# Kernel tuning notes

Measured on AMD Instinct MI355X. Metric: run time of the kernel, lower is better.

The kernel has to match this reference:

```python
import jax, jax.numpy as jnp
import numpy as np

ALPHA = 1.5      # entmax parameter from __init__
N_ITER = 50      # bisection iterations (converges well past fp32 precision)


def entmax_bisect(x, alpha=ALPHA, n_iter=N_ITER):
    """alpha-entmax along the last axis via bisection on the threshold tau.
    p_i = ((alpha-1)*x_i - tau)_+ ** (1/(alpha-1)), with sum_i p_i = 1.
    """
    q = 1.0 / (alpha - 1.0)
    z = x * (alpha - 1.0)
    mx = jnp.max(z, axis=-1, keepdims=True)
    # tau is bracketed by [mx - 1, mx]: sum >= 1 at lo, sum = 0 at hi
    lo, hi = mx - 1.0, mx

    def body(_, carry):
        lo, hi = carry
        tau = 0.5 * (lo + hi)
        f = jnp.sum(jnp.maximum(z - tau, 0.0) ** q, axis=-1, keepdims=True) - 1.0
        lo = jnp.where(f > 0.0, tau, lo)
        hi = jnp.where(f > 0.0, hi, tau)
        return lo, hi

    lo, hi = jax.lax.fori_loop(0, n_iter, body, (lo, hi))
    tau = 0.5 * (lo + hi)
    p = jnp.maximum(z - tau, 0.0) ** q
    return p / jnp.sum(p, axis=-1, keepdims=True)  # exact renormalization


def setup_inputs() -> dict:
    key = jax.random.key(0)
    kq, kk, kv = jax.random.split(key, 3)
    B, T, D = 16, 2048, 256
    return {
        "query": jax.random.normal(kq, (B, T, D), dtype=jnp.float32),
        "value": jax.random.normal(kv, (B, T, D), dtype=jnp.float32),
        "key": jax.random.normal(kk, (B, T, D), dtype=jnp.float32),
    }


def reference(query, value, key):
    # scores: [B, Tq, Tk]
    scores = jnp.einsum("btd,bsd->bts", query, key)
    weights = entmax_bisect(scores)          # sparse attention weights
    return jnp.einsum("bts,bsd->btd", weights, value)
```

## Files before the change

kernel.cpp:

```cpp
#include <hip/hip_runtime.h>

#define TT 2048
#define DD 256
#define RQB 128
#define NT 512
#define KB 128
#define NTILE (TT / KB)
#define NITER 30
#define CAP 28

#define L_CIDX 131072
#define L_CVAL (L_CIDX + RQB * CAP * 2)
#define L_CNT  (L_CVAL + RQB * CAP * 4)
#define L_SLOT (L_CNT + RQB * 4)
#define L_OVF  (L_SLOT + 8 * 16 * CAP * 2)
#define LDS_SZ (L_OVF + 16)

typedef __attribute__((ext_vector_type(4))) float f32x4;
typedef __attribute__((ext_vector_type(8))) short short8;

__device__ inline unsigned short f2bf(float x) {
    unsigned u = __float_as_uint(x);
    return (unsigned short)((u + 0x7fffu + ((u >> 16) & 1u)) >> 16);
}
__device__ inline float bf2f(unsigned short h) {
    return __uint_as_float((unsigned)h << 16);
}

__device__ __forceinline__ void gload16(const void* g, void* l) {
    __builtin_amdgcn_global_load_lds(
        (const __attribute__((address_space(1))) void*)g,
        (__attribute__((address_space(3))) void*)l, 16, 0, 0);
}

__device__ __forceinline__ float dppmax16(float m) {
    int a = __builtin_amdgcn_update_dpp(__float_as_int(m), __float_as_int(m),
                                        0xB1, 0xF, 0xF, false);
    m = fmaxf(m, __int_as_float(a));
    a = __builtin_amdgcn_update_dpp(__float_as_int(m), __float_as_int(m),
                                    0x4E, 0xF, 0xF, false);
    m = fmaxf(m, __int_as_float(a));
    a = __builtin_amdgcn_update_dpp(__float_as_int(m), __float_as_int(m),
                                    0x141, 0xF, 0xF, false);
    m = fmaxf(m, __int_as_float(a));
    a = __builtin_amdgcn_update_dpp(__float_as_int(m), __float_as_int(m),
                                    0x140, 0xF, 0xF, false);
    m = fmaxf(m, __int_as_float(a));
    return m;
}

__global__ __launch_bounds__(256) void split_k_kernel(const float* __restrict__ K,
        unsigned short* __restrict__ Kh, int n4) {
    int i = blockIdx.x * 256 + threadIdx.x;
    const int stride = gridDim.x * 256;
    for (; i < n4; i += stride) {
        float4 v = ((const float4*)K)[i];
        unsigned short h0 = f2bf(0.5f * v.x), h1 = f2bf(0.5f * v.y);
        unsigned short h2 = f2bf(0.5f * v.z), h3 = f2bf(0.5f * v.w);
        uint2 hv;
        hv.x = (unsigned)h0 | ((unsigned)h1 << 16);
        hv.y = (unsigned)h2 | ((unsigned)h3 << 16);
        ((uint2*)Kh)[i] = hv;
    }
}

__launch_bounds__(NT, 2)
__global__ void entmax_screen_kernel(const float* __restrict__ Q,
                                     const unsigned short* __restrict__ Kh,
                                     const float* __restrict__ Kf,
                                     const float* __restrict__ V,
                                     float* __restrict__ Out,
                                     int nwg) {
    extern __shared__ char smem[];
    unsigned short* CIDX = (unsigned short*)(smem + L_CIDX);
    float*          CVAL = (float*)(smem + L_CVAL);
    int*            CNT  = (int*)(smem + L_CNT);
    unsigned short* SLOT = (unsigned short*)(smem + L_SLOT);
    int*            POVF = (int*)(smem + L_OVF);

    const int tid = threadIdx.x;
    const int wid = tid >> 6, lane = tid & 63;
    const int l15 = lane & 15, ag = lane >> 4;
    const int wrow0 = wid * 16;

    const int lb = (blockIdx.x & 7) * (nwg >> 3) + (blockIdx.x >> 3);
    const int b  = lb >> 4;
    const int t0 = (lb & 15) * RQB;

    const char* KhB = (const char*)(Kh + (size_t)b * TT * DD);

    if (tid == 0) *POVF = 0;

    short8 ah[8];
    {
        const float* qr = Q + (size_t)(b * TT + t0 + wrow0 + l15) * DD;
        #pragma unroll
        for (int kk = 0; kk < 8; ++kk) {
            const int d0 = kk * 32 + ag * 8;
            float4 qa = *(const float4*)(qr + d0);
            float4 qb = *(const float4*)(qr + d0 + 4);
            float qf[8] = {qa.x, qa.y, qa.z, qa.w, qb.x, qb.y, qb.z, qb.w};
            #pragma unroll
            for (int i = 0; i < 8; ++i) ah[kk][i] = (short)f2bf(qf[i]);
        }
    }

    auto STAGE = [&](int tile, int buf) {
        #pragma unroll
        for (int j = 0; j < 8; ++j) {
            const int ofs = wid * 8192 + j * 1024 + lane * 16;
            const int cl = ofs >> 9, wb = ofs & 511;
            const size_t gb = ((size_t)((tile << 7) + cl) << 9) +
                              (size_t)(wb ^ ((cl & 7) << 4));
            gload16(KhB + gb, smem + buf * 65536 + wid * 8192 + j * 1024);
        }
    };

    STAGE(0, 0);
    __syncthreads();

    const unsigned long long grpmask = 0xFFFFULL << (ag * 16);
    const unsigned long long lowmask = (lane == 0) ? 0ULL : ((~0ULL) >> (64 - lane));
    float rmax[4];
    int   base[4];
    #pragma unroll
    for (int r = 0; r < 4; ++r) { rmax[r] = -3.402823466e38f; base[r] = 0; }

    for (int t = 0; t < NTILE; ++t) {
        const int cur = t & 1;
        if (t + 1 < NTILE) STAGE(t + 1, cur ^ 1);
        f32x4 acc[8];
        #pragma unroll
        for (int ct = 0; ct < 8; ++ct)
            #pragma unroll
            for (int r = 0; r < 4; ++r) acc[ct][r] = 0.0f;
        #pragma unroll
        for (int kk = 0; kk < 8; ++kk) {
            short8 bh[8];
            #pragma unroll
            for (int ct = 0; ct < 8; ++ct)
                bh[ct] = *(const short8*)(smem + cur * 65536 + (ct * 16 + l15) * 512 +
                                          (((kk * 64) + ag * 16) ^ ((l15 & 7) << 4)));
            #pragma unroll
            for (int ct = 0; ct < 8; ++ct)
                acc[ct] = __builtin_amdgcn_mfma_f32_16x16x32_bf16(ah[kk], bh[ct], acc[ct], 0, 0, 0);
        }
        #pragma unroll
        for (int rg = 0; rg < 4; ++rg) {
            float m = acc[0][rg];
            #pragma unroll
            for (int ct = 1; ct < 8; ++ct) m = fmaxf(m, acc[ct][rg]);
            m = dppmax16(m);
            rmax[rg] = fmaxf(rmax[rg], m);
            const float thr = rmax[rg] - 1.6f;
            if (m > thr) {
                const int row = wrow0 + ag * 4 + rg;
                #pragma unroll
                for (int ct = 0; ct < 8; ++ct) {
                    const bool p = acc[ct][rg] > thr;
                    const unsigned long long ball = __ballot(p) & grpmask;
                    if (ball) {
                        const int rank = (int)__popcll(ball & lowmask);
                        if (p && base[rg] + rank < CAP)
                            CIDX[row * CAP + base[rg] + rank] =
                                (unsigned short)((t << 7) + ct * 16 + l15);
                        base[rg] += (int)__popcll(ball);
                    }
                }
            }
        }
        __syncthreads();
    }

    #pragma unroll
    for (int rg = 0; rg < 4; ++rg) {
        if (l15 == 0) {
            CNT[wrow0 + ag * 4 + rg] = base[rg];
            if (base[rg] > CAP) *POVF = 1;
        }
    }
    __syncthreads();

    int c = 0;
    if (lane < 16) {
        const int cc = CNT[wrow0 + lane];
        c = cc > CAP ? CAP : cc;
    }
    int x = c;
    #pragma unroll
    for (int off = 1; off < 16; off <<= 1) {
        const int v = __shfl_up(x, off);
        if ((lane & 15) >= off) x += v;
    }
    const int pfx = x - c;
    const int total = __shfl(x, 15);
    if (lane < 16)
        for (int i = 0; i < c; ++i)
            SLOT[wid * (16 * CAP) + pfx + i] = (unsigned short)((lane << 8) | i);
    __syncthreads();

    {
        const float* Qb = Q + (size_t)(b * TT + t0 + wrow0) * DD;
        const float* Kb = Kf + (size_t)b * TT * DD;
        for (int bs = 0; bs < total; bs += 8) {
            float4 qv[8], kv[8];
            int rl[8], ii[8];
            #pragma unroll
            for (int u = 0; u < 8; ++u) {
                const int s = bs + u;
                const int e = (s < total) ? (int)SLOT[wid * (16 * CAP) + s] : 0;
                rl[u] = e >> 8; ii[u] = e & 255;
                const int col = (s < total) ? (int)CIDX[(wrow0 + rl[u]) * CAP + ii[u]] : 0;
                qv[u] = *(const float4*)(Qb + (size_t)rl[u] * DD + lane * 4);
                kv[u] = *(const float4*)(Kb + (size_t)col * DD + lane * 4);
            }
            float sm[8];
            #pragma unroll
            for (int u = 0; u < 8; ++u) {
                float d = qv[u].x * kv[u].x;
                d = fmaf(qv[u].y, kv[u].y, d);
                d = fmaf(qv[u].z, kv[u].z, d);
                d = fmaf(qv[u].w, kv[u].w, d);
                sm[u] = d;
            }
            #pragma unroll
            for (int off = 32; off; off >>= 1)
                #pragma unroll
                for (int u = 0; u < 8; ++u) sm[u] += __shfl_xor(sm[u], off);
            #pragma unroll
            for (int u = 0; u < 8; ++u)
                if (lane == u && bs + u < total)
                    CVAL[(wrow0 + rl[u]) * CAP + ii[u]] = 0.5f * sm[u];
        }
    }
    __syncthreads();

    if (*POVF) {
        if (wid == 0) {
            float* fbz = (float*)smem;
            for (int r = 0; r < RQB; ++r) {
                if (CNT[r] <= CAP) continue;
                const float* qr = Q + (size_t)(b * TT + t0 + r) * DD;
                const float* Kb = Kf + (size_t)b * TT * DD;
                for (int cc2 = lane; cc2 < TT; cc2 += 64) {
                    const float* kr = Kb + (size_t)cc2 * DD;
                    float a = 0.0f;
                    for (int d = 0; d < DD; ++d) a = fmaf(qr[d], kr[d], a);
                    fbz[cc2] = 0.5f * a;
                }
                __threadfence_block();
                float m = -3.402823466e38f;
                for (int cc2 = lane; cc2 < TT; cc2 += 64) m = fmaxf(m, fbz[cc2]);
                #pragma unroll
                for (int off = 32; off; off >>= 1) m = fmaxf(m, __shfl_xor(m, off));
                float lo = m - 1.0f, hi = m, tau;
                for (int it = 0; it < NITER; ++it) {
                    tau = 0.5f * (lo + hi);
                    float s = 0.0f;
                    for (int cc2 = lane; cc2 < TT; cc2 += 64) {
                        const float tt2 = fmaxf(fbz[cc2] - tau, 0.0f);
                        s = fmaf(tt2, tt2, s);
                    }
                    #pragma unroll
                    for (int off = 32; off; off >>= 1) s += __shfl_xor(s, off);
                    const bool gt = s > 1.0f;
                    lo = gt ? tau : lo;
                    hi = gt ? hi : tau;
                }
                tau = 0.5f * (lo + hi);
                float ssum = 0.0f;
                for (int cc2 = lane; cc2 < TT; cc2 += 64) {
                    const float tt2 = fmaxf(fbz[cc2] - tau, 0.0f);
                    ssum = fmaf(tt2, tt2, ssum);
                }
                #pragma unroll
                for (int off = 32; off; off >>= 1) ssum += __shfl_xor(ssum, off);
                const float inv = 1.0f / ssum;
                const int d4 = lane * 4;
                float4 o = make_float4(0.f, 0.f, 0.f, 0.f);
                for (int s = 0; s < TT; ++s) {
                    const float tt2 = fmaxf(fbz[s] - tau, 0.0f);
                    const float w = tt2 * tt2 * inv;
                    if (w > 0.0f) {
                        const float4 v = *(const float4*)(V + ((size_t)b * TT + s) * DD + d4);
                        o.x = fmaf(w, v.x, o.x); o.y = fmaf(w, v.y, o.y);
                        o.z = fmaf(w, v.z, o.z); o.w = fmaf(w, v.w, o.w);
                    }
                }
                *(float4*)(Out + ((size_t)(b * TT + t0 + r)) * DD + d4) = o;
                if (lane == 0) CNT[r] = -1;
                __threadfence_block();
            }
        }
        __syncthreads();
    }

    {
        const int myrow = wrow0 + (lane & 15);
        const int nRaw = CNT[myrow];
        const int n = (nRaw < 0) ? 0 : (nRaw > CAP ? CAP : nRaw);
        float cvr[CAP];
        #pragma unroll
        for (int i = 0; i < CAP; ++i)
            cvr[i] = (i < n) ? CVAL[myrow * CAP + i] : -3.0e30f;
        float emax = cvr[0];
        #pragma unroll
        for (int i = 1; i < CAP; ++i) emax = fmaxf(emax, cvr[i]);
        float lo = emax - 1.0f, hi = emax;
        for (int it = 0; it < NITER; ++it) {
            const float tau = 0.5f * (lo + hi);
            float s = 0.0f;
            #pragma unroll
            for (int i = 0; i < CAP; ++i) {
                const float tt2 = fmaxf(cvr[i] - tau, 0.0f);
                s = fmaf(tt2, tt2, s);
            }
            const bool gt = s > 1.0f;
            lo = gt ? tau : lo;
            hi = gt ? hi : tau;
        }
        const float tau = 0.5f * (lo + hi);
        float ssum = 0.0f;
        #pragma unroll
        for (int i = 0; i < CAP; ++i) {
            const float tt2 = fmaxf(cvr[i] - tau, 0.0f);
            ssum = fmaf(tt2, tt2, ssum);
        }
        const float inv = 1.0f / ssum;
        if (lane < 16 && n > 0) {
            for (int i = 0; i < n; ++i) {
                const float tt2 = fmaxf(cvr[i] - tau, 0.0f);
                CVAL[myrow * CAP + i] = tt2 * tt2 * inv;
            }
        }
    }

    const float* Vb = V + (size_t)b * TT * DD;
    for (int j = 0; j < 16; ++j) {
        const int row = wrow0 + j;
        const int n = CNT[row];
        if (n < 0) continue;
        const int d4 = lane * 4;
        float4 o = make_float4(0.f, 0.f, 0.f, 0.f);
        for (int i = 0; i < n; ++i) {
            const float wi = CVAL[row * CAP + i];
            if (wi > 0.0f) {
                const int si = (int)CIDX[row * CAP + i];
                const float4 v = *(const float4*)(Vb + (size_t)si * DD + d4);
                o.x = fmaf(wi, v.x, o.x); o.y = fmaf(wi, v.y, o.y);
                o.z = fmaf(wi, v.z, o.z); o.w = fmaf(wi, v.w, o.w);
            }
        }
        *(float4*)(Out + ((size_t)(b * TT + t0 + row)) * DD + d4) = o;
    }
}

#define DOT4(A, Kv, Qv) \
    A = fmaf((Qv).x, (Kv).x, fmaf((Qv).y, (Kv).y, fmaf((Qv).z, (Kv).z, fmaf((Qv).w, (Kv).w, (A)))))

__launch_bounds__(256, 2)
__global__ void entmax_fallback_kernel(const float* __restrict__ Q,
                                       const float* __restrict__ V,
                                       const float* __restrict__ K,
                                       float* __restrict__ Out) {
    extern __shared__ float zshf[];
    const int tid = threadIdx.x;
    const int b   = blockIdx.x >> 8;
    const int t0  = (blockIdx.x & 255) * 8;
    const float* Qb = Q + ((size_t)b * TT + t0) * DD;
    const float* Kb = K + (size_t)b * TT * DD;
    const float* Vb = V + (size_t)b * TT * DD;
    for (int g = 0; g < 2; ++g) {
        const int c0 = (g << 10) + tid;
        const float* k0 = Kb + (size_t)c0 * DD;
        float4 acc[8];
        #pragma unroll
        for (int r = 0; r < 8; ++r) acc[r] = make_float4(0.f, 0.f, 0.f, 0.f);
        for (int d = 0; d < DD; d += 4) {
            const float4 ka = *(const float4*)(k0 + d);
            const float4 kb = *(const float4*)(k0 + 256 * DD + d);
            const float4 kc = *(const float4*)(k0 + 512 * DD + d);
            const float4 kd = *(const float4*)(k0 + 768 * DD + d);
            #pragma unroll
            for (int r = 0; r < 8; ++r) {
                const float4 qv = *(const float4*)(Qb + r * DD + d);
                DOT4(acc[r].x, ka, qv); DOT4(acc[r].y, kb, qv);
                DOT4(acc[r].z, kc, qv); DOT4(acc[r].w, kd, qv);
            }
        }
        #pragma unroll
        for (int r = 0; r < 8; ++r) {
            zshf[r * TT + c0      ] = 0.5f * acc[r].x;
            zshf[r * TT + c0 + 256] = 0.5f * acc[r].y;
            zshf[r * TT + c0 + 512] = 0.5f * acc[r].z;
            zshf[r * TT + c0 + 768] = 0.5f * acc[r].w;
        }
    }
    __syncthreads();
    {
        const int wid = tid >> 6, lane = tid & 63;
        for (int rr = 0; rr < 2; ++rr) {
            const int r = wid * 2 + rr;
            float* z = zshf + r * TT;
            float zv[32];
            float m = -3.402823466e38f;
            #pragma unroll
            for (int j = 0; j < 32; ++j) { zv[j] = z[lane + (j << 6)]; m = fmaxf(m, zv[j]); }
            #pragma unroll
            for (int off = 32; off; off >>= 1) m = fmaxf(m, __shfl_xor(m, off));
            float lo = m - 1.0f, hi = m;
            for (int it = 0; it < NITER; ++it) {
                const float tau = 0.5f * (lo + hi);
                float s = 0.f;
                #pragma unroll
                for (int j = 0; j < 32; ++j) { float t = fmaxf(zv[j] - tau, 0.f); s = fmaf(t, t, s); }
                #pragma unroll
                for (int off = 32; off; off >>= 1) s += __shfl_xor(s, off);
                const bool gt = (s - 1.0f) > 0.0f;
                lo = gt ? tau : lo; hi = gt ? hi : tau;
            }
            const float tau = 0.5f * (lo + hi);
            float ssum = 0.f;
            #pragma unroll
            for (int j = 0; j < 32; ++j) { float t = fmaxf(zv[j] - tau, 0.f); ssum = fmaf(t, t, ssum); }
            #pragma unroll
            for (int off = 32; off; off >>= 1) ssum += __shfl_xor(ssum, off);
            const float inv = 1.0f / ssum;
            #pragma unroll
            for (int j = 0; j < 32; ++j) {
                float t = fmaxf(zv[j] - tau, 0.f);
                z[lane + (j << 6)] = t * t * inv;
            }
        }
    }
    __syncthreads();
    {
        const int d2 = (tid & 127) * 2;
        const int sg = tid >> 7;
        float2 acc[8];
        #pragma unroll
        for (int r = 0; r < 8; ++r) acc[r] = make_float2(0.f, 0.f);
        for (int sc = 0; sc < TT; sc += 8) {
            const int s0 = sc + sg * 4;
            float4 w4[8];
            #pragma unroll
            for (int r = 0; r < 8; ++r) w4[r] = *(const float4*)&zshf[r * TT + s0];
            #pragma unroll
            for (int js = 0; js < 4; ++js) {
                const float2 v = *(const float2*)(Vb + (size_t)(s0 + js) * DD + d2);
                #pragma unroll
                for (int r = 0; r < 8; ++r) {
                    const float wv = (js == 0) ? w4[r].x : (js == 1) ? w4[r].y
                                   : (js == 2) ? w4[r].z : w4[r].w;
                    acc[r].x = fmaf(wv, v.x, acc[r].x);
                    acc[r].y = fmaf(wv, v.y, acc[r].y);
                }
            }
        }
        __syncthreads();
        float* part = zshf;
        if (sg == 1) {
            #pragma unroll
            for (int r = 0; r < 8; ++r) *(float2*)&part[r * DD + d2] = acc[r];
        }
        __syncthreads();
        if (sg == 0) {
            #pragma unroll
            for (int r = 0; r < 8; ++r) {
                const float2 p = *(const float2*)&part[r * DD + d2];
                float2 o; o.x = acc[r].x + p.x; o.y = acc[r].y + p.y;
                *(float2*)&Out[((size_t)b * TT + t0 + r) * DD + d2] = o;
            }
        }
    }
}

extern "C" void kernel_launch(void* const* d_in, const int* in_sizes, int n_in,
                              void* d_out, int out_size, void* d_ws, size_t ws_size,
                              hipStream_t stream) {
    const float* Q = (const float*)d_in[0];
    const float* V = (const float*)d_in[1];
    const float* K = (const float*)d_in[2];
    float* Out = (float*)d_out;
    const int B = in_sizes[0] / (TT * DD);
    const size_t NE = (size_t)B * TT * DD;
    const size_t need = NE * 2;

    if (ws_size < need) {
        entmax_fallback_kernel<<<dim3(B * (TT / 8)), 256, 8 * TT * sizeof(float), stream>>>(
            Q, V, K, Out);
        return;
    }

    unsigned short* Kh = (unsigned short*)d_ws;
    split_k_kernel<<<2048, 256, 0, stream>>>(K, Kh, (int)(NE / 4));

    const int nwg = B * (TT / RQB);
    (void)hipFuncSetAttribute((const void*)entmax_screen_kernel,
                              hipFuncAttributeMaxDynamicSharedMemorySize, LDS_SZ);
    entmax_screen_kernel<<<dim3(nwg), NT, LDS_SZ, stream>>>(Q, Kh, K, V, Out, nwg);
}
```

Baseline: 135.0 us.

## Shrink workgroups to 32 query rows and 32-key tiles with precomputed LDS addressing

Cuts each workgroup from 128 query rows and 8 waves to 32 rows and 2 waves, with 32-key K tiles, so the grid has four times as many workgroups. The inner score loop now keeps two MFMA accumulators instead of eight. Global and LDS staging offsets and swizzled read pointers are computed once, before the loop. This aims for finer-grained scheduling and lower register and LDS pressure, but each workgroup still streams all of K, so total K traffic through L2 and the number of barriers per row rise.

```diff
diff --git a/kernel.cpp b/kernel.cpp
--- a/kernel.cpp
+++ b/kernel.cpp
@@ -2,18 +2,18 @@
 
 #define TT 2048
 #define DD 256
-#define RQB 128
-#define NT 512
-#define KB 128
+#define RQB 32
+#define NT 128
+#define KB 32
 #define NTILE (TT / KB)
 #define NITER 30
 #define CAP 28
 
-#define L_CIDX 131072
+#define L_CIDX 32768
 #define L_CVAL (L_CIDX + RQB * CAP * 2)
 #define L_CNT  (L_CVAL + RQB * CAP * 4)
 #define L_SLOT (L_CNT + RQB * 4)
-#define L_OVF  (L_SLOT + 8 * 16 * CAP * 2)
+#define L_OVF  (L_SLOT + 2 * 16 * CAP * 2)
 #define LDS_SZ (L_OVF + 16)
 
 typedef __attribute__((ext_vector_type(4))) float f32x4;
@@ -84,8 +84,8 @@
     const int wrow0 = wid * 16;
 
     const int lb = (blockIdx.x & 7) * (nwg >> 3) + (blockIdx.x >> 3);
-    const int b  = lb >> 4;
-    const int t0 = (lb & 15) * RQB;
+    const int b  = lb >> 6;
+    const int t0 = (lb & 63) * RQB;
 
     const char* KhB = (const char*)(Kh + (size_t)b * TT * DD);
 
@@ -105,18 +105,22 @@
         }
     }
 
-    auto STAGE = [&](int tile, int buf) {
-        #pragma unroll
-        for (int j = 0; j < 8; ++j) {
-            const int ofs = wid * 8192 + j * 1024 + lane * 16;
-            const int cl = ofs >> 9, wb = ofs & 511;
-            const size_t gb = ((size_t)((tile << 7) + cl) << 9) +
-                              (size_t)(wb ^ ((cl & 7) << 4));
-            gload16(KhB + gb, smem + buf * 65536 + wid * 8192 + j * 1024);
-        }
-    };
-
-    STAGE(0, 0);
+    int gofs[8], lofs[8];
+    #pragma unroll
+    for (int j = 0; j < 8; ++j) {
+        const int ofs = wid * 8192 + j * 1024 + lane * 16;
+        const int cl = ofs >> 9, wb = ofs & 511;
+        gofs[j] = cl * 512 + (wb ^ ((cl & 7) << 4));
+        lofs[j] = ofs;
+    }
+
+    const int sw = (l15 & 7) << 4;
+    const int qb_ = l15 * 512 + ((ag * 16) ^ (sw & 0x30));
+    const char* pE = smem + qb_ + (sw & 0x40);
+    const char* pO = smem + qb_ + (64 ^ (sw & 0x40));
+
+    #pragma unroll
+    for (int j = 0; j < 8; ++j) gload16(KhB + gofs[j], smem + lofs[j]);
     __syncthreads();
 
     const unsigned long long grpmask = 0xFFFFULL << (ag * 16);
@@ -128,42 +132,52 @@
 
     for (int t = 0; t < NTILE; ++t) {
         const int cur = t & 1;
-        if (t + 1 < NTILE) STAGE(t + 1, cur ^ 1);
-        f32x4 acc[8];
-        #pragma unroll
-        for (int ct = 0; ct < 8; ++ct)
-            #pragma unroll
-            for (int r = 0; r < 4; ++r) acc[ct][r] = 0.0f;
+        if (t + 1 < NTILE) {
+            const size_t gt = (size_t)(t + 1) * 16384;
+            const int lb_ = (cur ^ 1) * 16384;
+            #pragma unroll
+            for (int j = 0; j < 8; ++j)
+                gload16(KhB + gt + gofs[j], smem + lb_ + lofs[j]);
+        }
+        const char* pEc = pE + cur * 16384;
+        const char* pOc = pO + cur * 16384;
+        f32x4 acc0, acc1;
+        #pragma unroll
+        for (int r = 0; r < 4; ++r) { acc0[r] = 0.0f; acc1[r] = 0.0f; }
         #pragma unroll
         for (int kk = 0; kk < 8; ++kk) {
-            short8 bh[8];
-            #pragma unroll
-            for (int ct = 0; ct < 8; ++ct)
-                bh[ct] = *(const short8*)(smem + cur * 65536 + (ct * 16 + l15) * 512 +
-                                          (((kk * 64) + ag * 16) ^ ((l15 & 7) << 4)));
-            #pragma unroll
-            for (int ct = 0; ct < 8; ++ct)
-                acc[ct] = __builtin_amdgcn_mfma_f32_16x16x32_bf16(ah[kk], bh[ct], acc[ct], 0, 0, 0);
+            const char* pk = (kk & 1) ? pOc : pEc;
+            const short8 b0 = *(const short8*)(pk + (kk >> 1) * 128);
+            const short8 b1 = *(const short8*)(pk + 8192 + (kk >> 1) * 128);
+            acc0 = __builtin_amdgcn_mfma_f32_16x16x32_bf16(ah[kk], b0, acc0, 0, 0, 0);
+            acc1 = __builtin_amdgcn_mfma_f32_16x16x32_bf16(ah[kk], b1, acc1, 0, 0, 0);
         }
         #pragma unroll
         for (int rg = 0; rg < 4; ++rg) {
-            float m = acc[0][rg];
-            #pragma unroll
-            for (int ct = 1; ct < 8; ++ct) m = fmaxf(m, acc[ct][rg]);
-            m = dppmax16(m);
+            float m = dppmax16(fmaxf(acc0[rg], acc1[rg]));
             rmax[rg] = fmaxf(rmax[rg], m);
             const float thr = rmax[rg] - 1.6f;
             if (m > thr) {
                 const int row = wrow0 + ag * 4 + rg;
-                #pragma unroll
-                for (int ct = 0; ct < 8; ++ct) {
-                    const bool p = acc[ct][rg] > thr;
+                {
+                    const bool p = acc0[rg] > thr;
                     const unsigned long long ball = __ballot(p) & grpmask;
                     if (ball) {
                         const int rank = (int)__popcll(ball & lowmask);
                         if (p && base[rg] + rank < CAP)
                             CIDX[row * CAP + base[rg] + rank] =
-                                (unsigned short)((t << 7) + ct * 16 + l15);
+                                (unsigned short)((t << 5) + l15);
+                        base[rg] += (int)__popcll(ball);
+                    }
+                }
+                {
+                    const bool p = acc1[rg] > thr;
+                    const unsigned long long ball = __ballot(p) & grpmask;
+                    if (ball) {
+                        const int rank = (int)__popcll(ball & lowmask);
+                        if (p && base[rg] + rank < CAP)
+                            CIDX[row * CAP + base[rg] + rank] =
+                                (unsigned short)((t << 5) + 16 + l15);
                         base[rg] += (int)__popcll(ball);
                     }
                 }
```

Result: slower. 463.7 us (+243.5%).

## Split key columns across waves and screen candidates in two barrier-free passes

Applied to the files above, without the earlier changes.

Replaces the tile loop, in which all waves share double-buffered LDS K tiles with a barrier per tile, by a scheme where Q is staged once in LDS and each wave owns 256 key columns, reading K straight from global into registers. A first pass computes per-row maxima, which are reduced across waves into exact thresholds. A second pass recomputes the scores and collects candidates into per-wave lists (CAPW=6) that are then merged into the row list (CAP=24). This removes the 16 per-tile barriers and the running-max threshold, at the cost of computing QK^T twice. Tighter per-wave caps send more rows to the overflow path.

```diff
diff --git a/kernel.cpp b/kernel.cpp
--- a/kernel.cpp
+++ b/kernel.cpp
@@ -4,12 +4,16 @@
 #define DD 256
 #define RQB 128
 #define NT 512
-#define KB 128
-#define NTILE (TT / KB)
 #define NITER 30
-#define CAP 28
-
-#define L_CIDX 131072
+#define CAPW 6
+#define CAP 24
+#define THR_SLACK 1.75f
+
+#define L_GP   65536
+#define L_THR  (L_GP + 4096)
+#define L_CW   (L_THR + 512)
+#define L_IW   (L_CW + 4096)
+#define L_CIDX (L_IW + 8 * 128 * CAPW * 2)
 #define L_CVAL (L_CIDX + RQB * CAP * 2)
 #define L_CNT  (L_CVAL + RQB * CAP * 4)
 #define L_SLOT (L_CNT + RQB * 4)
@@ -25,12 +29,6 @@
 }
 __device__ inline float bf2f(unsigned short h) {
     return __uint_as_float((unsigned)h << 16);
-}
-
-__device__ __forceinline__ void gload16(const void* g, void* l) {
-    __builtin_amdgcn_global_load_lds(
-        (const __attribute__((address_space(1))) void*)g,
-        (__attribute__((address_space(3))) void*)l, 16, 0, 0);
 }
 
 __device__ __forceinline__ float dppmax16(float m) {
@@ -65,13 +63,17 @@
 }
 
 __launch_bounds__(NT, 2)
-__global__ void entmax_screen_kernel(const float* __restrict__ Q,
-                                     const unsigned short* __restrict__ Kh,
-                                     const float* __restrict__ Kf,
-                                     const float* __restrict__ V,
-                                     float* __restrict__ Out,
-                                     int nwg) {
+__global__ void entmax_nobar_kernel(const float* __restrict__ Q,
+                                    const unsigned short* __restrict__ Kh,
+                                    const float* __restrict__ Kf,
+                                    const float* __restrict__ V,
+                                    float* __restrict__ Out,
+                                    int nwg) {
     extern __shared__ char smem[];
+    float*          GP   = (float*)(smem + L_GP);
+    float*          THR  = (float*)(smem + L_THR);
+    int*            CW   = (int*)(smem + L_CW);
+    unsigned short* IW   = (unsigned short*)(smem + L_IW);
     unsigned short* CIDX = (unsigned short*)(smem + L_CIDX);
     float*          CVAL = (float*)(smem + L_CVAL);
     int*            CNT  = (int*)(smem + L_CNT);
@@ -89,102 +91,173 @@
 
     const char* KhB = (const char*)(Kh + (size_t)b * TT * DD);
 
+    ((int*)(smem + L_CW))[tid] = 0;
+    ((int*)(smem + L_CW))[tid + 512] = 0;
     if (tid == 0) *POVF = 0;
 
-    short8 ah[8];
     {
-        const float* qr = Q + (size_t)(b * TT + t0 + wrow0 + l15) * DD;
-        #pragma unroll
-        for (int kk = 0; kk < 8; ++kk) {
-            const int d0 = kk * 32 + ag * 8;
-            float4 qa = *(const float4*)(qr + d0);
-            float4 qb = *(const float4*)(qr + d0 + 4);
-            float qf[8] = {qa.x, qa.y, qa.z, qa.w, qb.x, qb.y, qb.z, qb.w};
-            #pragma unroll
-            for (int i = 0; i < 8; ++i) ah[kk][i] = (short)f2bf(qf[i]);
-        }
-    }
-
-    auto STAGE = [&](int tile, int buf) {
+        const int qrow = tid >> 2, seg = tid & 3;
+        const float* qsrc = Q + (size_t)(b * TT + t0 + qrow) * DD + seg * 64;
+        char* qd = smem + qrow * 512;
+        const int swr = (qrow & 7) << 4;
         #pragma unroll
         for (int j = 0; j < 8; ++j) {
-            const int ofs = wid * 8192 + j * 1024 + lane * 16;
-            const int cl = ofs >> 9, wb = ofs & 511;
-            const size_t gb = ((size_t)((tile << 7) + cl) << 9) +
-                              (size_t)(wb ^ ((cl & 7) << 4));
-            gload16(KhB + gb, smem + buf * 65536 + wid * 8192 + j * 1024);
-        }
-    };
-
-    STAGE(0, 0);
+            float4 f0 = *(const float4*)(qsrc + j * 8);
+            float4 f1 = *(const float4*)(qsrc + j * 8 + 4);
+            uint4 pk;
+            pk.x = (unsigned)f2bf(f0.x) | ((unsigned)f2bf(f0.y) << 16);
+            pk.y = (unsigned)f2bf(f0.z) | ((unsigned)f2bf(f0.w) << 16);
+            pk.z = (unsigned)f2bf(f1.x) | ((unsigned)f2bf(f1.y) << 16);
+            pk.w = (unsigned)f2bf(f1.z) | ((unsigned)f2bf(f1.w) << 16);
+            *(uint4*)(qd + ((seg * 128 + j * 16) ^ swr)) = pk;
+        }
+    }
     __syncthreads();
 
     const unsigned long long grpmask = 0xFFFFULL << (ag * 16);
     const unsigned long long lowmask = (lane == 0) ? 0ULL : ((~0ULL) >> (64 - lane));
-    float rmax[4];
-    int   base[4];
+    const int colw0 = wid * 256;
+    const int sx = (l15 & 7) << 4;
+    const char* qbase = smem + l15 * 512;
+
+    float mr[32];
     #pragma unroll
-    for (int r = 0; r < 4; ++r) { rmax[r] = -3.402823466e38f; base[r] = 0; }
-
-    for (int t = 0; t < NTILE; ++t) {
-        const int cur = t & 1;
-        if (t + 1 < NTILE) STAGE(t + 1, cur ^ 1);
-        f32x4 acc[8];
-        #pragma unroll
-        for (int ct = 0; ct < 8; ++ct)
-            #pragma unroll
-            for (int r = 0; r < 4; ++r) acc[ct][r] = 0.0f;
-        #pragma unroll
-        for (int kk = 0; kk < 8; ++kk) {
-            short8 bh[8];
-            #pragma unroll
-            for (int ct = 0; ct < 8; ++ct)
-                bh[ct] = *(const short8*)(smem + cur * 65536 + (ct * 16 + l15) * 512 +
-                                          (((kk * 64) + ag * 16) ^ ((l15 & 7) << 4)));
-            #pragma unroll
-            for (int ct = 0; ct < 8; ++ct)
-                acc[ct] = __builtin_amdgcn_mfma_f32_16x16x32_bf16(ah[kk], bh[ct], acc[ct], 0, 0, 0);
-        }
-        #pragma unroll
-        for (int rg = 0; rg < 4; ++rg) {
-            float m = acc[0][rg];
-            #pragma unroll
-            for (int ct = 1; ct < 8; ++ct) m = fmaxf(m, acc[ct][rg]);
-            m = dppmax16(m);
-            rmax[rg] = fmaxf(rmax[rg], m);
-            const float thr = rmax[rg] - 1.6f;
-            if (m > thr) {
-                const int row = wrow0 + ag * 4 + rg;
-                #pragma unroll
-                for (int ct = 0; ct < 8; ++ct) {
-                    const bool p = acc[ct][rg] > thr;
-                    const unsigned long long ball = __ballot(p) & grpmask;
-                    if (ball) {
-                        const int rank = (int)__popcll(ball & lowmask);
-                        if (p && base[rg] + rank < CAP)
-                            CIDX[row * CAP + base[rg] + rank] =
-                                (unsigned short)((t << 7) + ct * 16 + l15);
-                        base[rg] += (int)__popcll(ball);
+    for (int i = 0; i < 32; ++i) mr[i] = -3.0e30f;
+
+    for (int tc = 0; tc < 8; ++tc) {
+        const char* kb0 = KhB + (size_t)(colw0 + tc * 32 + l15) * 512 + ag * 16;
+        short8 Bf[2][8];
+        #pragma unroll
+        for (int ct = 0; ct < 2; ++ct)
+            #pragma unroll
+            for (int kk = 0; kk < 8; ++kk)
+                Bf[ct][kk] = *(const short8*)(kb0 + ct * 8192 + kk * 64);
+        #pragma unroll
+        for (int rp = 0; rp < 4; ++rp) {
+            f32x4 acc[2][2];
+            #pragma unroll
+            for (int rg = 0; rg < 2; ++rg)
+                #pragma unroll
+                for (int ct = 0; ct < 2; ++ct)
+                    #pragma unroll
+                    for (int r = 0; r < 4; ++r) acc[rg][ct][r] = 0.0f;
+            #pragma unroll
+            for (int kk = 0; kk < 8; ++kk) {
+                const int kb = (kk * 64 + ag * 16) ^ sx;
+                short8 a0 = *(const short8*)(qbase + (rp * 32) * 512 + kb);
+                short8 a1 = *(const short8*)(qbase + (rp * 32 + 16) * 512 + kb);
+                acc[0][0] = __builtin_amdgcn_mfma_f32_16x16x32_bf16(a0, Bf[0][kk], acc[0][0], 0, 0, 0);
+                acc[0][1] = __builtin_amdgcn_mfma_f32_16x16x32_bf16(a0, Bf[1][kk], acc[0][1], 0, 0, 0);
+                acc[1][0] = __builtin_amdgcn_mfma_f32_16x16x32_bf16(a1, Bf[0][kk], acc[1][0], 0, 0, 0);
+                acc[1][1] = __builtin_amdgcn_mfma_f32_16x16x32_bf16(a1, Bf[1][kk], acc[1][1], 0, 0, 0);
+            }
+            #pragma unroll
+            for (int rg = 0; rg < 2; ++rg)
+                #pragma unroll
+                for (int r = 0; r < 4; ++r)
+                    mr[rp * 8 + rg * 4 + r] = fmaxf(mr[rp * 8 + rg * 4 + r],
+                                                    fmaxf(acc[rg][0][r], acc[rg][1][r]));
+        }
+    }
+    #pragma unroll
+    for (int rp = 0; rp < 4; ++rp)
+        #pragma unroll
+        for (int rg = 0; rg < 2; ++rg)
+            #pragma unroll
+            for (int r = 0; r < 4; ++r) {
+                const float m = dppmax16(mr[rp * 8 + rg * 4 + r]);
+                if (l15 == 0)
+                    GP[wid * 128 + rp * 32 + rg * 16 + ag * 4 + r] = m;
+            }
+    __syncthreads();
+    if (tid < 128) {
+        float m = GP[tid];
+        #pragma unroll
+        for (int w = 1; w < 8; ++w) m = fmaxf(m, GP[w * 128 + tid]);
+        THR[tid] = m - THR_SLACK;
+    }
+    __syncthreads();
+
+    #pragma unroll
+    for (int rp = 0; rp < 4; ++rp)
+        #pragma unroll
+        for (int rg = 0; rg < 2; ++rg)
+            #pragma unroll
+            for (int r = 0; r < 4; ++r)
+                mr[rp * 8 + rg * 4 + r] = THR[rp * 32 + rg * 16 + ag * 4 + r];
+
+    for (int tc = 0; tc < 8; ++tc) {
+        const char* kb0 = KhB + (size_t)(colw0 + tc * 32 + l15) * 512 + ag * 16;
+        short8 Bf[2][8];
+        #pragma unroll
+        for (int ct = 0; ct < 2; ++ct)
+            #pragma unroll
+            for (int kk = 0; kk < 8; ++kk)
+                Bf[ct][kk] = *(const short8*)(kb0 + ct * 8192 + kk * 64);
+        #pragma unroll
+        for (int rp = 0; rp < 4; ++rp) {
+            f32x4 acc[2][2];
+            #pragma unroll
+            for (int rg = 0; rg < 2; ++rg)
+                #pragma unroll
+                for (int ct = 0; ct < 2; ++ct)
+                    #pragma unroll
+                    for (int r = 0; r < 4; ++r) acc[rg][ct][r] = 0.0f;
+            #pragma unroll
+            for (int kk = 0; kk < 8; ++kk) {
+                const int kb = (kk * 64 + ag * 16) ^ sx;
+                short8 a0 = *(const short8*)(qbase + (rp * 32) * 512 + kb);
+                short8 a1 = *(const short8*)(qbase + (rp * 32 + 16) * 512 + kb);
+                acc[0][0] = __builtin_amdgcn_mfma_f32_16x16x32_bf16(a0, Bf[0][kk], acc[0][0], 0, 0, 0);
+                acc[0][1] = __builtin_amdgcn_mfma_f32_16x16x32_bf16(a0, Bf[1][kk], acc[0][1], 0, 0, 0);
+                acc[1][0] = __builtin_amdgcn_mfma_f32_16x16x32_bf16(a1, Bf[0][kk], acc[1][0], 0, 0, 0);
+                acc[1][1] = __builtin_amdgcn_mfma_f32_16x16x32_bf16(a1, Bf[1][kk], acc[1][1], 0, 0, 0);
+            }
+            #pragma unroll
+            for (int rg = 0; rg < 2; ++rg)
+                #pragma unroll
+                for (int r = 0; r < 4; ++r) {
+                    const float thrv = mr[rp * 8 + rg * 4 + r];
+                    const int row = rp * 32 + rg * 16 + ag * 4 + r;
+                    #pragma unroll
+                    for (int ct = 0; ct < 2; ++ct) {
+                        const bool p = acc[rg][ct][r] > thrv;
+                        const unsigned long long ball = __ballot(p) & grpmask;
+                        if (ball) {
+                            const int cnt = (int)__popcll(ball);
+                            const int rank = (int)__popcll(ball & lowmask);
+                            const int base = CW[wid * 128 + row];
+                            if (p && base + rank < CAPW)
+                                IW[(wid * 128 + row) * CAPW + base + rank] =
+                                    (unsigned short)(colw0 + tc * 32 + ct * 16 + l15);
+                            if (l15 == 0) CW[wid * 128 + row] = base + cnt;
+                        }
                     }
                 }
-            }
-        }
-        __syncthreads();
-    }
-
-    #pragma unroll
-    for (int rg = 0; rg < 4; ++rg) {
-        if (l15 == 0) {
-            CNT[wrow0 + ag * 4 + rg] = base[rg];
-            if (base[rg] > CAP) *POVF = 1;
-        }
-    }
-    __syncthreads();
+        }
+    }
+    __syncthreads();
+
+    if (lane < 16) {
+        const int row = wrow0 + lane;
+        int n = 0, ovf = 0;
+        for (int w = 0; w < 8; ++w) {
+            int cw = CW[w * 128 + row];
+            if (cw > CAPW) { ovf = 1; cw = CAPW; }
+            for (int i = 0; i < cw; ++i) {
+                if (n < CAP) CIDX[row * CAP + n] = IW[(w * 128 + row) * CAPW + i];
+                ++n;
+            }
+        }
+        if (n > CAP) ovf = 1;
+        CNT[row] = ovf ? (CAP + 1) : n;
+        if (ovf) *POVF = 1;
+    }
 
     int c = 0;
     if (lane < 16) {
         const int cc = CNT[wrow0 + lane];
-        c = cc > CAP ? CAP : cc;
+        c = (cc > CAP) ? 0 : cc;
     }
     int x = c;
     #pragma unroll
@@ -197,7 +270,6 @@
     if (lane < 16)
         for (int i = 0; i < c; ++i)
             SLOT[wid * (16 * CAP) + pfx + i] = (unsigned short)((lane << 8) | i);
-    __syncthreads();
 
     {
         const float* Qb = Q + (size_t)(b * TT + t0 + wrow0) * DD;
@@ -298,7 +370,7 @@
     {
         const int myrow = wrow0 + (lane & 15);
         const int nRaw = CNT[myrow];
-        const int n = (nRaw < 0) ? 0 : (nRaw > CAP ? CAP : nRaw);
+        const int n = (nRaw < 0 || nRaw > CAP) ? 0 : nRaw;
         float cvr[CAP];
         #pragma unroll
         for (int i = 0; i < CAP; ++i)
@@ -339,7 +411,7 @@
     for (int j = 0; j < 16; ++j) {
         const int row = wrow0 + j;
         const int n = CNT[row];
-        if (n < 0) continue;
+        if (n < 0 || n > CAP) continue;
         const int d4 = lane * 4;
         float4 o = make_float4(0.f, 0.f, 0.f, 0.f);
         for (int i = 0; i < n; ++i) {
@@ -496,7 +568,7 @@
     split_k_kernel<<<2048, 256, 0, stream>>>(K, Kh, (int)(NE / 4));
 
     const int nwg = B * (TT / RQB);
-    (void)hipFuncSetAttribute((const void*)entmax_screen_kernel,
+    (void)hipFuncSetAttribute((const void*)entmax_nobar_kernel,
                               hipFuncAttributeMaxDynamicSharedMemorySize, LDS_SZ);
-    entmax_screen_kernel<<<dim3(nwg), NT, LDS_SZ, stream>>>(Q, Kh, K, V, Out, nwg);
-}
+    entmax_nobar_kernel<<<dim3(nwg), NT, LDS_SZ, stream>>>(Q, Kh, K, V, Out, nwg);
+}
```

After: 198.1 us. +46.8%, slower.

## Pack K in MFMA fragment layout and stream it from global directly into registers

Applied to the files above, without the earlier changes.

The K bf16 pre-pass now writes K in the exact per-lane MFMA B-fragment order, so the screening kernel loads B operands straight from global/L2 into registers. This drops the LDS double-buffered staging and its per-tile barriers. Work is regrouped so each wave covers 32 query rows over half the key columns, reusing each B fragment for two A fragments, and per-wave candidate lists are merged into a larger per-row CAP. It frees a large amount of LDS and removes synchronization, at the cost of more global/L2 traffic per wave and larger candidate buffers.

```diff
diff --git a/kernel.cpp b/kernel.cpp
--- a/kernel.cpp
+++ b/kernel.cpp
@@ -4,12 +4,15 @@
 #define DD 256
 #define RQB 128
 #define NT 512
-#define KB 128
-#define NTILE (TT / KB)
 #define NITER 30
-#define CAP 28
-
-#define L_CIDX 131072
+#define CAPW 24
+#define CAP 48
+#define SLACK 1.6f
+
+#define L_FBZ  0
+#define L_CW   8192
+#define L_IW   (L_CW + 1024)
+#define L_CIDX (L_IW + 8 * 32 * CAPW * 2)
 #define L_CVAL (L_CIDX + RQB * CAP * 2)
 #define L_CNT  (L_CVAL + RQB * CAP * 4)
 #define L_SLOT (L_CNT + RQB * 4)
@@ -22,15 +25,6 @@
 __device__ inline unsigned short f2bf(float x) {
     unsigned u = __float_as_uint(x);
     return (unsigned short)((u + 0x7fffu + ((u >> 16) & 1u)) >> 16);
-}
-__device__ inline float bf2f(unsigned short h) {
-    return __uint_as_float((unsigned)h << 16);
-}
-
-__device__ __forceinline__ void gload16(const void* g, void* l) {
-    __builtin_amdgcn_global_load_lds(
-        (const __attribute__((address_space(1))) void*)g,
-        (__attribute__((address_space(3))) void*)l, 16, 0, 0);
 }
 
 __device__ __forceinline__ float dppmax16(float m) {
@@ -49,29 +43,48 @@
     return m;
 }
 
-__global__ __launch_bounds__(256) void split_k_kernel(const float* __restrict__ K,
-        unsigned short* __restrict__ Kh, int n4) {
-    int i = blockIdx.x * 256 + threadIdx.x;
-    const int stride = gridDim.x * 256;
-    for (; i < n4; i += stride) {
-        float4 v = ((const float4*)K)[i];
-        unsigned short h0 = f2bf(0.5f * v.x), h1 = f2bf(0.5f * v.y);
-        unsigned short h2 = f2bf(0.5f * v.z), h3 = f2bf(0.5f * v.w);
-        uint2 hv;
-        hv.x = (unsigned)h0 | ((unsigned)h1 << 16);
-        hv.y = (unsigned)h2 | ((unsigned)h3 << 16);
-        ((uint2*)Kh)[i] = hv;
-    }
+__global__ __launch_bounds__(256) void pack_k_kernel(const float* __restrict__ K,
+        unsigned short* __restrict__ Khf) {
+    const int t = blockIdx.x * 256 + threadIdx.x;
+    const int lane = t & 63;
+    const int kk = (t >> 6) & 7;
+    const int g  = (t >> 9) & 127;
+    const int b  = t >> 16;
+    const int col = g * 16 + (lane & 15);
+    const int d0  = kk * 32 + (lane >> 4) * 8;
+    const float* src = K + ((size_t)b * TT + col) * DD + d0;
+    const float4 f0 = *(const float4*)(src);
+    const float4 f1 = *(const float4*)(src + 4);
+    uint4 pk;
+    pk.x = (unsigned)f2bf(0.5f * f0.x) | ((unsigned)f2bf(0.5f * f0.y) << 16);
+    pk.y = (unsigned)f2bf(0.5f * f0.z) | ((unsigned)f2bf(0.5f * f0.w) << 16);
+    pk.z = (unsigned)f2bf(0.5f * f1.x) | ((unsigned)f2bf(0.5f * f1.y) << 16);
+    pk.w = (unsigned)f2bf(0.5f * f1.z) | ((unsigned)f2bf(0.5f * f1.w) << 16);
+    *(uint4*)(Khf + (size_t)t * 8) = pk;
 }
 
+#define LOADB(B_, g_) do { \
+    _Pragma("unroll") for (int kk_ = 0; kk_ < 8; ++kk_) \
+        B_[kk_] = *(const short8*)(KfB + ((size_t)((Gbase + (g_)) * 8 + kk_) << 10) + lane * 16); \
+    } while (0)
+
+#define PROCF(B_, aA_, aB_) do { \
+    _Pragma("unroll") for (int r_ = 0; r_ < 4; ++r_) { aA_[r_] = 0.0f; aB_[r_] = 0.0f; } \
+    _Pragma("unroll") for (int kk_ = 0; kk_ < 8; ++kk_) { \
+        aA_ = __builtin_amdgcn_mfma_f32_16x16x32_bf16(ah0[kk_], B_[kk_], aA_, 0, 0, 0); \
+        aB_ = __builtin_amdgcn_mfma_f32_16x16x32_bf16(ah1[kk_], B_[kk_], aB_, 0, 0, 0); \
+    } } while (0)
+
 __launch_bounds__(NT, 2)
-__global__ void entmax_screen_kernel(const float* __restrict__ Q,
-                                     const unsigned short* __restrict__ Kh,
-                                     const float* __restrict__ Kf,
-                                     const float* __restrict__ V,
-                                     float* __restrict__ Out,
-                                     int nwg) {
+__global__ void entmax_frag_kernel(const float* __restrict__ Q,
+                                   const unsigned short* __restrict__ Khf,
+                                   const float* __restrict__ Kf,
+                                   const float* __restrict__ V,
+                                   float* __restrict__ Out,
+                                   int nwg) {
     extern __shared__ char smem[];
+    int*            CW   = (int*)(smem + L_CW);
+    unsigned short* IW   = (unsigned short*)(smem + L_IW);
     unsigned short* CIDX = (unsigned short*)(smem + L_CIDX);
     float*          CVAL = (float*)(smem + L_CVAL);
     int*            CNT  = (int*)(smem + L_CNT);
@@ -81,110 +94,124 @@
     const int tid = threadIdx.x;
     const int wid = tid >> 6, lane = tid & 63;
     const int l15 = lane & 15, ag = lane >> 4;
+    const int rg = wid >> 1, cg = wid & 1;
     const int wrow0 = wid * 16;
 
     const int lb = (blockIdx.x & 7) * (nwg >> 3) + (blockIdx.x >> 3);
     const int b  = lb >> 4;
     const int t0 = (lb & 15) * RQB;
 
-    const char* KhB = (const char*)(Kh + (size_t)b * TT * DD);
-
+    const char* KfB = (const char*)Khf + (size_t)b * 1048576;
+    const int Gbase = cg * 64;
+    const int colw0 = cg * 1024;
+
+    if (lane < 32) CW[wid * 32 + lane] = 0;
     if (tid == 0) *POVF = 0;
 
-    short8 ah[8];
+    short8 ah0[8], ah1[8];
     {
-        const float* qr = Q + (size_t)(b * TT + t0 + wrow0 + l15) * DD;
+        const float* q0 = Q + (size_t)(b * TT + t0 + rg * 32 + l15) * DD;
+        const float* q1 = q0 + 16 * DD;
         #pragma unroll
         for (int kk = 0; kk < 8; ++kk) {
             const int d0 = kk * 32 + ag * 8;
-            float4 qa = *(const float4*)(qr + d0);
-            float4 qb = *(const float4*)(qr + d0 + 4);
-            float qf[8] = {qa.x, qa.y, qa.z, qa.w, qb.x, qb.y, qb.z, qb.w};
-            #pragma unroll
-            for (int i = 0; i < 8; ++i) ah[kk][i] = (short)f2bf(qf[i]);
-        }
-    }
-
-    auto STAGE = [&](int tile, int buf) {
-        #pragma unroll
-        for (int j = 0; j < 8; ++j) {
-            const int ofs = wid * 8192 + j * 1024 + lane * 16;
-            const int cl = ofs >> 9, wb = ofs & 511;
-            const size_t gb = ((size_t)((tile << 7) + cl) << 9) +
-                              (size_t)(wb ^ ((cl & 7) << 4));
-            gload16(KhB + gb, smem + buf * 65536 + wid * 8192 + j * 1024);
-        }
-    };
-
-    STAGE(0, 0);
-    __syncthreads();
+            float4 a = *(const float4*)(q0 + d0);
+            float4 c = *(const float4*)(q0 + d0 + 4);
+            float qf[8] = {a.x, a.y, a.z, a.w, c.x, c.y, c.z, c.w};
+            #pragma unroll
+            for (int i = 0; i < 8; ++i) ah0[kk][i] = (short)f2bf(qf[i]);
+            a = *(const float4*)(q1 + d0);
+            c = *(const float4*)(q1 + d0 + 4);
+            float qg[8] = {a.x, a.y, a.z, a.w, c.x, c.y, c.z, c.w};
+            #pragma unroll
+            for (int i = 0; i < 8; ++i) ah1[kk][i] = (short)f2bf(qg[i]);
+        }
+    }
 
     const unsigned long long grpmask = 0xFFFFULL << (ag * 16);
     const unsigned long long lowmask = (lane == 0) ? 0ULL : ((~0ULL) >> (64 - lane));
-    float rmax[4];
-    int   base[4];
+    float rm0[4], rm1[4];
+    int   bs0[4], bs1[4];
     #pragma unroll
-    for (int r = 0; r < 4; ++r) { rmax[r] = -3.402823466e38f; base[r] = 0; }
-
-    for (int t = 0; t < NTILE; ++t) {
-        const int cur = t & 1;
-        if (t + 1 < NTILE) STAGE(t + 1, cur ^ 1);
-        f32x4 acc[8];
-        #pragma unroll
-        for (int ct = 0; ct < 8; ++ct)
-            #pragma unroll
-            for (int r = 0; r < 4; ++r) acc[ct][r] = 0.0f;
-        #pragma unroll
-        for (int kk = 0; kk < 8; ++kk) {
-            short8 bh[8];
-            #pragma unroll
-            for (int ct = 0; ct < 8; ++ct)
-                bh[ct] = *(const short8*)(smem + cur * 65536 + (ct * 16 + l15) * 512 +
-                                          (((kk * 64) + ag * 16) ^ ((l15 & 7) << 4)));
-            #pragma unroll
-            for (int ct = 0; ct < 8; ++ct)
-                acc[ct] = __builtin_amdgcn_mfma_f32_16x16x32_bf16(ah[kk], bh[ct], acc[ct], 0, 0, 0);
-        }
-        #pragma unroll
-        for (int rg = 0; rg < 4; ++rg) {
-            float m = acc[0][rg];
-            #pragma unroll
-            for (int ct = 1; ct < 8; ++ct) m = fmaxf(m, acc[ct][rg]);
+    for (int r = 0; r < 4; ++r) {
+        rm0[r] = -3.0e30f; rm1[r] = -3.0e30f;
+        bs0[r] = 0; bs1[r] = 0;
+    }
+
+    auto screen4 = [&](float (&rm)[4], int (&bs)[4], int fof,
+                       const f32x4& x0, const f32x4& x1,
+                       const f32x4& x2, const f32x4& x3, int c0) {
+        #pragma unroll
+        for (int r = 0; r < 4; ++r) {
+            float m = fmaxf(fmaxf(x0[r], x1[r]), fmaxf(x2[r], x3[r]));
             m = dppmax16(m);
-            rmax[rg] = fmaxf(rmax[rg], m);
-            const float thr = rmax[rg] - 1.6f;
+            rm[r] = fmaxf(rm[r], m);
+            const float thr = rm[r] - SLACK;
             if (m > thr) {
-                const int row = wrow0 + ag * 4 + rg;
-                #pragma unroll
-                for (int ct = 0; ct < 8; ++ct) {
-                    const bool p = acc[ct][rg] > thr;
-                    const unsigned long long ball = __ballot(p) & grpmask;
-                    if (ball) {
-                        const int rank = (int)__popcll(ball & lowmask);
-                        if (p && base[rg] + rank < CAP)
-                            CIDX[row * CAP + base[rg] + rank] =
-                                (unsigned short)((t << 7) + ct * 16 + l15);
-                        base[rg] += (int)__popcll(ball);
+                const int lrow = wid * 32 + fof + ag * 4 + r;
+                const float vals[4] = {x0[r], x1[r], x2[r], x3[r]};
+                #pragma unroll
+                for (int ch = 0; ch < 4; ++ch) {
+                    const bool p = vals[ch] > thr;
+                    const unsigned long long ba = __ballot(p) & grpmask;
+                    if (ba) {
+                        const int rk = (int)__popcll(ba & lowmask);
+                        if (p && bs[r] + rk < CAPW)
+                            IW[lrow * CAPW + bs[r] + rk] =
+                                (unsigned short)(colw0 + (c0 + ch) * 16 + l15);
+                        bs[r] += (int)__popcll(ba);
                     }
                 }
             }
         }
-        __syncthreads();
-    }
-
-    #pragma unroll
-    for (int rg = 0; rg < 4; ++rg) {
-        if (l15 == 0) {
-            CNT[wrow0 + ag * 4 + rg] = base[rg];
-            if (base[rg] > CAP) *POVF = 1;
-        }
+    };
+
+    short8 B0[8], B1[8];
+    for (int j = 0; j < 16; ++j) {
+        const int c0 = j * 4;
+        f32x4 a0A, a0B, a1A, a1B, a2A, a2B, a3A, a3B;
+        LOADB(B0, c0);
+        LOADB(B1, c0 + 1);
+        PROCF(B0, a0A, a0B);
+        LOADB(B0, c0 + 2);
+        PROCF(B1, a1A, a1B);
+        LOADB(B1, c0 + 3);
+        PROCF(B0, a2A, a2B);
+        PROCF(B1, a3A, a3B);
+        screen4(rm0, bs0, 0,  a0A, a1A, a2A, a3A, c0);
+        screen4(rm1, bs1, 16, a0B, a1B, a2B, a3B, c0);
+    }
+
+    if (l15 == 0) {
+        #pragma unroll
+        for (int r = 0; r < 4; ++r) {
+            CW[wid * 32 + ag * 4 + r]      = bs0[r];
+            CW[wid * 32 + 16 + ag * 4 + r] = bs1[r];
+        }
+    }
+    __syncthreads();
+
+    if (lane < 16) {
+        const int row = wrow0 + lane;
+        const int lr = row & 31;
+        const int w0 = (row >> 5) * 2;
+        int n = 0, ovf = 0;
+        #pragma unroll
+        for (int wv = 0; wv < 2; ++wv) {
+            int cw = CW[(w0 + wv) * 32 + lr];
+            if (cw > CAPW) { ovf = 1; cw = CAPW; }
+            for (int i = 0; i < cw; ++i)
+                CIDX[row * CAP + (n++)] = IW[((w0 + wv) * 32 + lr) * CAPW + i];
+        }
+        CNT[row] = ovf ? (CAP + 1) : n;
+        if (ovf) *POVF = 1;
     }
     __syncthreads();
 
     int c = 0;
     if (lane < 16) {
         const int cc = CNT[wrow0 + lane];
-        c = cc > CAP ? CAP : cc;
+        c = (cc > CAP) ? 0 : cc;
     }
     int x = c;
     #pragma unroll
@@ -197,17 +224,16 @@
     if (lane < 16)
         for (int i = 0; i < c; ++i)
             SLOT[wid * (16 * CAP) + pfx + i] = (unsigned short)((lane << 8) | i);
-    __syncthreads();
 
     {
         const float* Qb = Q + (size_t)(b * TT + t0 + wrow0) * DD;
         const float* Kb = Kf + (size_t)b * TT * DD;
-        for (int bs = 0; bs < total; bs += 8) {
+        for (int bsx = 0; bsx < total; bsx += 8) {
             float4 qv[8], kv[8];
             int rl[8], ii[8];
             #pragma unroll
             for (int u = 0; u < 8; ++u) {
-                const int s = bs + u;
+                const int s = bsx + u;
                 const int e = (s < total) ? (int)SLOT[wid * (16 * CAP) + s] : 0;
                 rl[u] = e >> 8; ii[u] = e & 255;
                 const int col = (s < total) ? (int)CIDX[(wrow0 + rl[u]) * CAP + ii[u]] : 0;
@@ -229,7 +255,7 @@
                 for (int u = 0; u < 8; ++u) sm[u] += __shfl_xor(sm[u], off);
             #pragma unroll
             for (int u = 0; u < 8; ++u)
-                if (lane == u && bs + u < total)
+                if (lane == u && bsx + u < total)
                     CVAL[(wrow0 + rl[u]) * CAP + ii[u]] = 0.5f * sm[u];
         }
     }
@@ -237,7 +263,7 @@
 
     if (*POVF) {
         if (wid == 0) {
-            float* fbz = (float*)smem;
+            float* fbz = (float*)(smem + L_FBZ);
             for (int r = 0; r < RQB; ++r) {
                 if (CNT[r] <= CAP) continue;
                 const float* qr = Q + (size_t)(b * TT + t0 + r) * DD;
@@ -298,7 +324,7 @@
     {
         const int myrow = wrow0 + (lane & 15);
         const int nRaw = CNT[myrow];
-        const int n = (nRaw < 0) ? 0 : (nRaw > CAP ? CAP : nRaw);
+        const int n = (nRaw < 0 || nRaw > CAP) ? 0 : nRaw;
         float cvr[CAP];
         #pragma unroll
         for (int i = 0; i < CAP; ++i)
@@ -339,7 +365,7 @@
     for (int j = 0; j < 16; ++j) {
         const int row = wrow0 + j;
         const int n = CNT[row];
-        if (n < 0) continue;
+        if (n < 0 || n > CAP) continue;
         const int d4 = lane * 4;
         float4 o = make_float4(0.f, 0.f, 0.f, 0.f);
         for (int i = 0; i < n; ++i) {
@@ -492,11 +518,11 @@
         return;
     }
 
-    unsigned short* Kh = (unsigned short*)d_ws;
-    split_k_kernel<<<2048, 256, 0, stream>>>(K, Kh, (int)(NE / 4));
+    unsigned short* Khf = (unsigned short*)d_ws;
+    pack_k_kernel<<<dim3(B * 256), 256, 0, stream>>>(K, Khf);
 
     const int nwg = B * (TT / RQB);
-    (void)hipFuncSetAttribute((const void*)entmax_screen_kernel,
+    (void)hipFuncSetAttribute((const void*)entmax_frag_kernel,
                               hipFuncAttributeMaxDynamicSharedMemorySize, LDS_SZ);
-    entmax_screen_kernel<<<dim3(nwg), NT, LDS_SZ, stream>>>(Q, Kh, K, V, Out, nwg);
+    entmax_frag_kernel<<<dim3(nwg), NT, LDS_SZ, stream>>>(Q, Khf, K, V, Out, nwg);
 }
```

New measurement: 174.6 us. +29.4%, slower.
